# Kernel optimization log

Measured on AMD Instinct MI355X. Metric: run time of the kernel, lower is better.

The kernel has to match this reference:

```python
import jax, jax.numpy as jnp
import numpy as np

B, T, I, H = 32, 1024, 512, 512


def setup_inputs() -> dict:
    key = jax.random.key(0)
    ks = jax.random.split(key, 9)
    s = 0.05  # xavier-ish scale for 512-dim layers
    return {
        "x": jax.random.normal(ks[0], (B, T, I), jnp.float32),
        "W_in_0": jax.random.normal(ks[1], (I, H), jnp.float32) * s,
        "b_in_0": jnp.zeros((H,), jnp.float32),
        "W_h_0": jax.random.normal(ks[2], (H, 2 * H), jnp.float32) * s,
        "b_h_0": jnp.zeros((2 * H,), jnp.float32),
        "W_in_1": jax.random.normal(ks[3], (H, H), jnp.float32) * s,
        "b_in_1": jnp.zeros((H,), jnp.float32),
        "W_h_1": jax.random.normal(ks[4], (H, 2 * H), jnp.float32) * s,
        "b_h_1": jnp.zeros((2 * H,), jnp.float32),
    }


def _cell(ti, m_prev, c_prev, W_h, b_h, hid):
    # ti: transformed input [B,H]; gates from previous m (the "hidden")
    gates = m_prev @ W_h + b_h                 # [B,2H]
    retain = jax.nn.sigmoid(gates[:, :hid])
    merge = jax.nn.sigmoid(gates[:, hid:])
    c_next = jnp.tanh(c_prev + retain * ti)
    m_next = (1.0 - merge) * ti + merge * c_next
    return m_next, c_next


def reference(x, W_in_0, b_in_0, W_h_0, b_h_0, W_in_1, b_in_1, W_h_1, b_h_1):
    b, t, _ = x.shape
    hid = W_in_0.shape[1]
    # layer-0 input transform is independent of the recurrence: batch it over time
    ti0_all = jnp.swapaxes(x @ W_in_0 + b_in_0, 0, 1)  # [T,B,H]

    def step(carry, ti0):
        (m0, c0), (m1, c1) = carry
        m0n, c0n = _cell(ti0, m0, c0, W_h_0, b_h_0, hid)
        ti1 = m0n @ W_in_1 + b_in_1
        m1n, c1n = _cell(ti1, m1, c1, W_h_1, b_h_1, hid)
        out_t = jnp.stack([m0n, m1n], axis=1)  # [B,L,H]
        return ((m0n, c0n), (m1n, c1n)), out_t

    z = jnp.zeros((b, hid), x.dtype)
    init = ((z, z), (z, z))
    (h0, h1), outs = jax.lax.scan(step, init, ti0_all)
    output = jnp.swapaxes(outs, 0, 1)  # [B,T,L,H]
    final_c = jnp.stack([h0[1], h1[1]], axis=1)  # [B,L,H]
    con = jnp.broadcast_to(final_c[:, None], output.shape)  # [B,T,L,H]
    return (output, output, con)
```

## Files before the change

### kernel.cpp

```cpp
#include <hip/hip_runtime.h>


#define T_STEPS 1024

typedef __bf16 bf8 __attribute__((ext_vector_type(8)));
typedef float  f4  __attribute__((ext_vector_type(4)));
typedef unsigned u32x4 __attribute__((ext_vector_type(4)));

__device__ __forceinline__ f4 mfma16(bf8 a, bf8 b, f4 c) {
    return __builtin_amdgcn_mfma_f32_16x16x32_bf16(a, b, c, 0, 0, 0);
}
__device__ __forceinline__ float sigf(float x)     { return 1.f / (1.f + __expf(-x)); }
__device__ __forceinline__ float tanhfast(float x) { return 1.f - 2.f / (1.f + __expf(2.f * x)); }
__device__ __forceinline__ unsigned pack2(float lo, float hi) {
    union { __bf16 h; unsigned short u; } a, b;
    a.h = (__bf16)lo; b.h = (__bf16)hi;
    return ((unsigned)b.u << 16) | (unsigned)a.u;
}
__device__ __forceinline__ void wait_lds_ge(int* p, int tgt) {
    while (__hip_atomic_load(p, __ATOMIC_ACQUIRE, __HIP_MEMORY_SCOPE_WORKGROUP) < tgt)
        __builtin_amdgcn_s_sleep(1);
}
__device__ __forceinline__ void set_lds(int* p, int v) {
    __hip_atomic_store(p, v, __ATOMIC_RELEASE, __HIP_MEMORY_SCOPE_WORKGROUP);
}
__device__ __forceinline__ void poll_flags(const unsigned* fbase, unsigned tgt, int lane) {
    while (true) {
        unsigned v = 0xFFFFFFFFu;
        if (lane < 32)
            v = __hip_atomic_load(fbase + lane * 16, __ATOMIC_RELAXED,
                                  __HIP_MEMORY_SCOPE_AGENT);
        if (__ballot(v >= tgt) == ~0ull) break;
        __builtin_amdgcn_s_sleep(1);
    }
    __builtin_amdgcn_sched_barrier(0);
}


__global__ __launch_bounds__(256) void k_init(const float* __restrict__ x,
                                              const float* __restrict__ w_in0,
                                              __bf16* __restrict__ xbf,
                                              __bf16* __restrict__ w0hi,
                                              __bf16* __restrict__ w0lo,
                                              unsigned* __restrict__ ws)
{
    size_t id = (size_t)blockIdx.x * 256 + threadIdx.x;
    size_t gs = (size_t)gridDim.x * 256;
    for (size_t i = id; i < 34816; i += gs) ws[i] = 0u;
    for (size_t i = id; i < (size_t)16777216; i += gs) {
        size_t r = i >> 9, c = i & 511;
        size_t b = r & 31, t = r >> 5;
        xbf[i] = (__bf16)x[(((b << 10) + t) << 9) + c];
    }
    for (size_t i = id; i < (size_t)262144; i += gs) {
        size_t n = i >> 9, k = i & 511;
        float v = w_in0[(k << 9) + n];
        __bf16 h = (__bf16)v;
        w0hi[i] = h;
        w0lo[i] = (__bf16)(v - (float)h);
    }
}

__global__ __launch_bounds__(256) void k_pregemm(const __bf16* __restrict__ xbf,
                                                 const __bf16* __restrict__ w0hi,
                                                 const __bf16* __restrict__ w0lo,
                                                 const float* __restrict__ b_in0,
                                                 float* __restrict__ ti0)
{
    int tid = threadIdx.x, lane = tid & 63, wid = tid >> 6;
    int wg = blockIdx.x;
    int mbase = (wg & 511) * 64 + wid * 16;
    int nbase = (wg >> 9) * 128;
    int col = lane & 15, kgrp = lane >> 4;
    f4 acc[8];
#pragma unroll
    for (int i = 0; i < 8; ++i) acc[i] = (f4){0.f, 0.f, 0.f, 0.f};
    const __bf16* ap = xbf + (size_t)(mbase + col) * 512 + kgrp * 8;
    for (int kk = 0; kk < 16; ++kk) {
        bf8 a = *reinterpret_cast<const bf8*>(ap + kk * 32);
        const __bf16* wb = w0hi + (size_t)(nbase + col) * 512 + kk * 32 + kgrp * 8;
        const __bf16* wl = w0lo + (size_t)(nbase + col) * 512 + kk * 32 + kgrp * 8;
#pragma unroll
        for (int ct = 0; ct < 8; ++ct) {
            bf8 bh = *reinterpret_cast<const bf8*>(wb + (size_t)ct * 16 * 512);
            bf8 bl = *reinterpret_cast<const bf8*>(wl + (size_t)ct * 16 * 512);
            acc[ct] = mfma16(a, bh, acc[ct]);
            acc[ct] = mfma16(a, bl, acc[ct]);
        }
    }
#pragma unroll
    for (int ct = 0; ct < 8; ++ct) {
        int c = nbase + ct * 16 + col;
        float bias = b_in0[c];
#pragma unroll
        for (int r = 0; r < 4; ++r) {
            int row = mbase + kgrp * 4 + r;
            ti0[(size_t)row * 512 + c] = acc[ct][r] + bias;
        }
    }
}

__global__ __launch_bounds__(192, 1) void k_recur(
    const float* __restrict__ wh0, const float* __restrict__ bh0g,
    const float* __restrict__ win1, const float* __restrict__ bin1g,
    const float* __restrict__ wh1, const float* __restrict__ bh1g,
    const float* __restrict__ ti0,
    float* __restrict__ out,
    unsigned* __restrict__ ws)
{
    __shared__ __bf16 sW[9][8192];
    __shared__ float  sTi1[2][256];
    __shared__ float  sMn0[2][256];
    __shared__ float  sMn1[2][256];
    __shared__ float  sB[5][16];
    __shared__ int    sAready, sAout, sB1rdy, sBdone, sCdone;

    int tid = threadIdx.x, lane = tid & 63, wid = tid >> 6;
    int wg = blockIdx.x;
    int rank  = wg & 31;
    int mhalf = wg >> 5;

    unsigned* flagsA = ws + mhalf * 512;
    unsigned* flagsB = ws + 1024 + mhalf * 512;
    unsigned* ring0d = ws + 2048;
    unsigned* ring1d = ws + 18432;
    float* fc = (float*)(ws + 34816);

    int h0 = rank * 16;
    int col = lane & 15, kgrp = lane >> 4;
    int rbrow = mhalf * 16;

    for (int i = tid; i < 8192; i += 192) {
        int cl = i & 15, k = i >> 4;
        int sw = (cl * 512 + k) ^ ((cl & 7) << 3);
        float v0r = wh0[(size_t)k * 1024 + h0 + cl];
        float v0m = wh0[(size_t)k * 1024 + 512 + h0 + cl];
        float v1r = wh1[(size_t)k * 1024 + h0 + cl];
        float v1m = wh1[(size_t)k * 1024 + 512 + h0 + cl];
        float vt  = win1[(size_t)k * 512 + h0 + cl];
        __bf16 a;
        a = (__bf16)v0r; sW[0][sw] = a; sW[1][sw] = (__bf16)(v0r - (float)a);
        a = (__bf16)v0m; sW[2][sw] = a; sW[3][sw] = (__bf16)(v0m - (float)a);
        a = (__bf16)v1r; sW[4][sw] = a; sW[5][sw] = (__bf16)(v1r - (float)a);
        a = (__bf16)v1m; sW[6][sw] = a; sW[7][sw] = (__bf16)(v1m - (float)a);
        sW[8][sw] = (__bf16)vt;
    }
    if (tid < 16) {
        sB[0][tid] = bh0g[h0 + tid];
        sB[1][tid] = bh0g[512 + h0 + tid];
        sB[2][tid] = bh1g[h0 + tid];
        sB[3][tid] = bh1g[512 + h0 + tid];
        sB[4][tid] = bin1g[h0 + tid];
    }
    if (tid == 0) { sAready = -1; sAout = -1; sB1rdy = -1; sBdone = -1; sCdone = -1; }
    __syncthreads();

    float cs[4] = {0.f, 0.f, 0.f, 0.f};

    if (wid == 0) {
#pragma unroll 1
        for (int ph = 0; ph <= T_STEPS; ++ph) {
            float t0v[4] = {0.f, 0.f, 0.f, 0.f};
            if (ph < T_STEPS) {
#pragma unroll
                for (int r = 0; r < 4; ++r)
                    t0v[r] = ti0[((size_t)ph * 32 + rbrow + kgrp * 4 + r) * 512 + h0 + col];
            }
            if (ph > 0) poll_flags(flagsA, (unsigned)ph, lane);
            u32x4 au[16];
            {
                const unsigned* rp = ring0d + ((ph + 1) & 1) * 8192
                                   + (rbrow + col) * 8 + (kgrp & 1) * 4;
#pragma unroll
                for (int kk = 0; kk < 16; ++kk)
                    asm volatile("global_load_dwordx4 %0, %1, off sc1"
                                 : "=v"(au[kk]) : "v"(rp + (2 * kk + (kgrp >> 1)) * 256));
            }
            f4 accR = {0.f, 0.f, 0.f, 0.f};
            f4 accM = {0.f, 0.f, 0.f, 0.f};
            f4 accT = {0.f, 0.f, 0.f, 0.f};
            asm volatile("s_waitcnt vmcnt(8)" ::: "memory");
            __builtin_amdgcn_sched_barrier(0);
#pragma unroll
            for (int kk = 0; kk < 8; ++kk) {
                union { u32x4 u; bf8 v; } A; A.u = au[kk];
                int e = (col * 512 + kk * 32 + kgrp * 8) ^ ((col & 7) << 3);
                accR = mfma16(A.v, *reinterpret_cast<const bf8*>(&sW[0][e]), accR);
                accR = mfma16(A.v, *reinterpret_cast<const bf8*>(&sW[1][e]), accR);
                accM = mfma16(A.v, *reinterpret_cast<const bf8*>(&sW[2][e]), accM);
                accM = mfma16(A.v, *reinterpret_cast<const bf8*>(&sW[3][e]), accM);
                accT = mfma16(A.v, *reinterpret_cast<const bf8*>(&sW[8][e]), accT);
            }
            asm volatile("s_waitcnt vmcnt(0)" ::: "memory");
            __builtin_amdgcn_sched_barrier(0);
#pragma unroll
            for (int kk = 8; kk < 16; ++kk) {
                union { u32x4 u; bf8 v; } A; A.u = au[kk];
                int e = (col * 512 + kk * 32 + kgrp * 8) ^ ((col & 7) << 3);
                accR = mfma16(A.v, *reinterpret_cast<const bf8*>(&sW[0][e]), accR);
                accR = mfma16(A.v, *reinterpret_cast<const bf8*>(&sW[1][e]), accR);
                accM = mfma16(A.v, *reinterpret_cast<const bf8*>(&sW[2][e]), accM);
                accM = mfma16(A.v, *reinterpret_cast<const bf8*>(&sW[3][e]), accM);
                accT = mfma16(A.v, *reinterpret_cast<const bf8*>(&sW[8][e]), accT);
            }
            wait_lds_ge(&sBdone, ph - 2);
#pragma unroll
            for (int r = 0; r < 4; ++r)
                sTi1[ph & 1][(kgrp * 4 + r) * 16 + col] = accT[r] + sB[4][col];
            if (lane == 0) set_lds(&sAready, ph);

            if (ph < T_STEPS) {
                float mn[4];
#pragma unroll
                for (int r = 0; r < 4; ++r) {
                    float retain = sigf(accR[r] + sB[0][col]);
                    float merge  = sigf(accM[r] + sB[1][col]);
                    float cv = tanhfast(cs[r] + retain * t0v[r]);
                    cs[r] = cv;
                    mn[r] = (1.f - merge) * t0v[r] + merge * cv;
                }
#pragma unroll
                for (int r = 0; r < 4; ++r) {
                    float hi = __shfl_xor(mn[r], 1, 64);
                    if (!(col & 1)) {
                        int row = rbrow + kgrp * 4 + r;
                        __hip_atomic_store(&ring0d[(ph & 1) * 8192 + rank * 256 + row * 8 + (col >> 1)],
                                           pack2(mn[r], hi), __ATOMIC_RELAXED,
                                           __HIP_MEMORY_SCOPE_AGENT);
                    }
                }
                asm volatile("s_waitcnt vmcnt(0)" ::: "memory");
                if (lane == 0)
                    __hip_atomic_store(&flagsA[rank * 16], (unsigned)(ph + 1), __ATOMIC_RELAXED,
                                       __HIP_MEMORY_SCOPE_AGENT);
                wait_lds_ge(&sCdone, ph - 2);
#pragma unroll
                for (int r = 0; r < 4; ++r)
                    sMn0[ph & 1][(kgrp * 4 + r) * 16 + col] = mn[r];
                if (lane == 0) set_lds(&sAout, ph);
            }
        }
#pragma unroll
        for (int r = 0; r < 4; ++r) {
            int b = rbrow + kgrp * 4 + r;
            fc[((size_t)b * 2 + 0) * 512 + h0 + col] = cs[r];
        }
    } else if (wid == 1) {
#pragma unroll 1
        for (int ph = 1; ph <= T_STEPS; ++ph) {
            if (ph >= 2) poll_flags(flagsB, (unsigned)(ph - 1), lane);
            u32x4 au[16];
            {
                const unsigned* rp = ring1d + (ph & 1) * 8192
                                   + (rbrow + col) * 8 + (kgrp & 1) * 4;
#pragma unroll
                for (int kk = 0; kk < 16; ++kk)
                    asm volatile("global_load_dwordx4 %0, %1, off sc1"
                                 : "=v"(au[kk]) : "v"(rp + (2 * kk + (kgrp >> 1)) * 256));
                asm volatile("s_waitcnt vmcnt(0)" ::: "memory");
                __builtin_amdgcn_sched_barrier(0);
            }
            f4 accR = {0.f, 0.f, 0.f, 0.f};
            f4 accM = {0.f, 0.f, 0.f, 0.f};
#pragma unroll
            for (int kk = 0; kk < 16; ++kk) {
                union { u32x4 u; bf8 v; } A; A.u = au[kk];
                int e = (col * 512 + kk * 32 + kgrp * 8) ^ ((col & 7) << 3);
                accR = mfma16(A.v, *reinterpret_cast<const bf8*>(&sW[4][e]), accR);
                accR = mfma16(A.v, *reinterpret_cast<const bf8*>(&sW[5][e]), accR);
                accM = mfma16(A.v, *reinterpret_cast<const bf8*>(&sW[6][e]), accM);
                accM = mfma16(A.v, *reinterpret_cast<const bf8*>(&sW[7][e]), accM);
            }
            wait_lds_ge(&sAready, ph);
            float t1v[4];
#pragma unroll
            for (int r = 0; r < 4; ++r)
                t1v[r] = sTi1[ph & 1][(kgrp * 4 + r) * 16 + col];
            if (lane == 0) set_lds(&sBdone, ph);
            float mn[4];
#pragma unroll
            for (int r = 0; r < 4; ++r) {
                float retain = sigf(accR[r] + sB[2][col]);
                float merge  = sigf(accM[r] + sB[3][col]);
                float cv = tanhfast(cs[r] + retain * t1v[r]);
                cs[r] = cv;
                mn[r] = (1.f - merge) * t1v[r] + merge * cv;
            }
#pragma unroll
            for (int r = 0; r < 4; ++r) {
                float hi = __shfl_xor(mn[r], 1, 64);
                if (!(col & 1)) {
                    int row = rbrow + kgrp * 4 + r;
                    __hip_atomic_store(&ring1d[((ph + 1) & 1) * 8192 + rank * 256 + row * 8 + (col >> 1)],
                                       pack2(mn[r], hi), __ATOMIC_RELAXED,
                                       __HIP_MEMORY_SCOPE_AGENT);
                }
            }
            asm volatile("s_waitcnt vmcnt(0)" ::: "memory");
            if (lane == 0)
                __hip_atomic_store(&flagsB[rank * 16], (unsigned)ph, __ATOMIC_RELAXED,
                                   __HIP_MEMORY_SCOPE_AGENT);
            wait_lds_ge(&sCdone, ph - 2);
#pragma unroll
            for (int r = 0; r < 4; ++r)
                sMn1[ph & 1][(kgrp * 4 + r) * 16 + col] = mn[r];
            if (lane == 0) set_lds(&sB1rdy, ph);
        }
#pragma unroll
        for (int r = 0; r < 4; ++r) {
            int b = rbrow + kgrp * 4 + r;
            fc[((size_t)b * 2 + 1) * 512 + h0 + col] = cs[r];
        }
    } else {
#pragma unroll 1
        for (int ph = 0; ph <= T_STEPS; ++ph) {
            float m0[4], m1[4];
            bool has0 = (ph < T_STEPS), has1 = (ph >= 1);
            if (has0) {
                wait_lds_ge(&sAout, ph);
#pragma unroll
                for (int r = 0; r < 4; ++r)
                    m0[r] = sMn0[ph & 1][(kgrp * 4 + r) * 16 + col];
            }
            if (has1) {
                wait_lds_ge(&sB1rdy, ph);
#pragma unroll
                for (int r = 0; r < 4; ++r)
                    m1[r] = sMn1[ph & 1][(kgrp * 4 + r) * 16 + col];
            }
            if (lane == 0) set_lds(&sCdone, ph);
            if (has0) {
#pragma unroll
                for (int r = 0; r < 4; ++r) {
                    int b = rbrow + kgrp * 4 + r;
                    size_t ob = ((size_t)b * 1024 + ph) * 1024 + h0 + col;
                    __builtin_nontemporal_store(m0[r], out + ob);
                    __builtin_nontemporal_store(m0[r], out + (size_t)33554432 + ob);
                }
            }
            if (has1) {
#pragma unroll
                for (int r = 0; r < 4; ++r) {
                    int b = rbrow + kgrp * 4 + r;
                    size_t ob = ((size_t)b * 1024 + (ph - 1)) * 1024 + 512 + h0 + col;
                    __builtin_nontemporal_store(m1[r], out + ob);
                    __builtin_nontemporal_store(m1[r], out + (size_t)33554432 + ob);
                }
            }
        }
    }
}

__global__ __launch_bounds__(256) void k_final(const float* __restrict__ fc,
                                               float* __restrict__ seg2)
{
    size_t id = (size_t)blockIdx.x * 256 + threadIdx.x;
    size_t gs = (size_t)gridDim.x * 256;
    for (size_t i = id; i < (size_t)8388608; i += gs) {
        size_t flat = i * 4;
        int h = (int)(flat & 511);
        int l = (int)((flat >> 9) & 1);
        int b = (int)(flat >> 20);
        f4 v = *reinterpret_cast<const f4*>(&fc[((size_t)b * 2 + l) * 512 + h]);
        *reinterpret_cast<f4*>(&seg2[flat]) = v;
    }
}

extern "C" void kernel_launch(void* const* d_in, const int* in_sizes, int n_in,
                              void* d_out, int out_size, void* d_ws, size_t ws_size,
                              hipStream_t stream)
{
    const float* x     = (const float*)d_in[0];
    const float* w_in0 = (const float*)d_in[1];
    const float* b_in0 = (const float*)d_in[2];
    const float* wh0   = (const float*)d_in[3];
    const float* bh0   = (const float*)d_in[4];
    const float* win1  = (const float*)d_in[5];
    const float* bin1  = (const float*)d_in[6];
    const float* wh1   = (const float*)d_in[7];
    const float* bh1   = (const float*)d_in[8];
    float* out = (float*)d_out;

    float*  seg2 = out + (size_t)2 * 33554432;
    float*  ti0  = seg2;
    __bf16* xbf  = (__bf16*)(ti0 + 16777216);
    __bf16* w0hi = xbf + 16777216;
    __bf16* w0lo = w0hi + 262144;

    k_init<<<1024, 256, 0, stream>>>(x, w_in0, xbf, w0hi, w0lo, (unsigned*)d_ws);
    k_pregemm<<<2048, 256, 0, stream>>>(xbf, w0hi, w0lo, b_in0, ti0);
    k_recur<<<64, 192, 0, stream>>>(wh0, bh0, win1, bin1, wh1, bh1, ti0, out,
                                    (unsigned*)d_ws);
    k_final<<<1024, 256, 0, stream>>>((const float*)((unsigned*)d_ws + 34816), seg2);
}
```

Measured before the change: 4.479 ms.

## Prefetch next-step inputs and flags, reorder layer-0 ring publish before LDS handoff

Wave 0 now prefetches the next timestep's transformed input with inline global loads issued after the ring store, so the load latency overlaps the flag-publish wait. It also speculatively loads the peer flags right after publishing its own, and uses a ballot over them to skip the polling loop when every peer is already ready. The m0 compute and ring publish are moved ahead of the sTi1 LDS handoff, shortening the cross-workgroup critical path. This adds fragile asm-level ordering with vmcnt waits and depends on the speculative flag read being fresh enough.

```diff
diff --git a/kernel.cpp b/kernel.cpp
--- a/kernel.cpp
+++ b/kernel.cpp
@@ -158,15 +158,23 @@
     float cs[4] = {0.f, 0.f, 0.f, 0.f};
 
     if (wid == 0) {
+        float t0n[4];
+#pragma unroll
+        for (int r = 0; r < 4; ++r)
+            asm volatile("global_load_dword %0, %1, off"
+                         : "=v"(t0n[r])
+                         : "v"(ti0 + ((size_t)(rbrow + kgrp * 4 + r)) * 512 + h0 + col));
+        unsigned pv = 0;
 #pragma unroll 1
         for (int ph = 0; ph <= T_STEPS; ++ph) {
-            float t0v[4] = {0.f, 0.f, 0.f, 0.f};
-            if (ph < T_STEPS) {
-#pragma unroll
-                for (int r = 0; r < 4; ++r)
-                    t0v[r] = ti0[((size_t)ph * 32 + rbrow + kgrp * 4 + r) * 512 + h0 + col];
-            }
-            if (ph > 0) poll_flags(flagsA, (unsigned)ph, lane);
+            if (ph > 0) {
+                asm volatile("s_waitcnt vmcnt(0)" ::: "memory");
+                __builtin_amdgcn_sched_barrier(0);
+                unsigned v = (lane < 32 && lane != rank) ? pv : 0xFFFFFFFFu;
+                if (__ballot(v >= (unsigned)ph) != ~0ull)
+                    poll_flags(flagsA, (unsigned)ph, lane);
+                __builtin_amdgcn_sched_barrier(0);
+            }
             u32x4 au[16];
             {
                 const unsigned* rp = ring0d + ((ph + 1) & 1) * 8192
@@ -203,21 +211,16 @@
                 accM = mfma16(A.v, *reinterpret_cast<const bf8*>(&sW[3][e]), accM);
                 accT = mfma16(A.v, *reinterpret_cast<const bf8*>(&sW[8][e]), accT);
             }
-            wait_lds_ge(&sBdone, ph - 2);
-#pragma unroll
-            for (int r = 0; r < 4; ++r)
-                sTi1[ph & 1][(kgrp * 4 + r) * 16 + col] = accT[r] + sB[4][col];
-            if (lane == 0) set_lds(&sAready, ph);
-
+
+            float mn[4];
             if (ph < T_STEPS) {
-                float mn[4];
 #pragma unroll
                 for (int r = 0; r < 4; ++r) {
                     float retain = sigf(accR[r] + sB[0][col]);
                     float merge  = sigf(accM[r] + sB[1][col]);
-                    float cv = tanhfast(cs[r] + retain * t0v[r]);
+                    float cv = tanhfast(cs[r] + retain * t0n[r]);
                     cs[r] = cv;
-                    mn[r] = (1.f - merge) * t0v[r] + merge * cv;
+                    mn[r] = (1.f - merge) * t0n[r] + merge * cv;
                 }
 #pragma unroll
                 for (int r = 0; r < 4; ++r) {
@@ -229,10 +232,29 @@
                                            __HIP_MEMORY_SCOPE_AGENT);
                     }
                 }
+                if (ph + 1 < T_STEPS) {
+#pragma unroll
+                    for (int r = 0; r < 4; ++r)
+                        asm volatile("global_load_dword %0, %1, off"
+                                     : "=v"(t0n[r])
+                                     : "v"(ti0 + ((size_t)(ph + 1) * 32 + rbrow + kgrp * 4 + r) * 512 + h0 + col));
+                }
                 asm volatile("s_waitcnt vmcnt(0)" ::: "memory");
                 if (lane == 0)
                     __hip_atomic_store(&flagsA[rank * 16], (unsigned)(ph + 1), __ATOMIC_RELAXED,
                                        __HIP_MEMORY_SCOPE_AGENT);
+                if (lane < 32 && lane != rank)
+                    asm volatile("global_load_dword %0, %1, off sc1"
+                                 : "=v"(pv) : "v"(flagsA + lane * 16));
+            }
+
+            wait_lds_ge(&sBdone, ph - 2);
+#pragma unroll
+            for (int r = 0; r < 4; ++r)
+                sTi1[ph & 1][(kgrp * 4 + r) * 16 + col] = accT[r] + sB[4][col];
+            if (lane == 0) set_lds(&sAready, ph);
+
+            if (ph < T_STEPS) {
                 wait_lds_ge(&sCdone, ph - 2);
 #pragma unroll
                 for (int r = 0; r < 4; ++r)
```

New measurement: 4.310 ms. 3.8% less time.
